# Optimization experiments

Hardware: AMD Instinct MI355X
Metric: run time of the kernel (lower is better)

Reference implementation:

```python
import jax, jax.numpy as jnp
import numpy as np

B, C, H, W = 4, 64, 512, 512
NS = 2048   # n_samples edges per image
NL = 1000   # number of superpixel labels


def setup_inputs() -> dict:
    key = jax.random.key(0)
    k1, k2, k3, k4 = jax.random.split(key, 4)
    x = jax.random.normal(k1, (B, C, H, W), dtype=jnp.float32)
    label_maps = jax.random.randint(k2, (B, 1, H, W), 0, NL).astype(jnp.int32)
    edges = jax.random.randint(k3, (B, NS, 2), 0, NL).astype(jnp.int32)
    edge_weights = (jax.random.uniform(k4, (B, NS)) > 0.5).astype(jnp.float32)
    return {"x": x, "label_maps": label_maps, "edges": edges,
            "edge_weights": edge_weights, "n_labels": NL}


def reference(x, label_maps, edges, edge_weights, n_labels):
    # x: [B,C,H,W]; label_maps: [B,1,H,W] int; edges: [B,NS,2] int; edge_weights: [B,NS]
    Bd, Cd, Hd, Wd = x.shape

    def per_image_means(xi, li):
        feats = xi.reshape(Cd, Hd * Wd).T            # [HW, C]
        lab = li.reshape(-1)                          # [HW]
        sums = jax.ops.segment_sum(feats, lab, num_segments=n_labels)   # [NL, C]
        cnts = jax.ops.segment_sum(jnp.ones((Hd * Wd,), xi.dtype), lab,
                                   num_segments=n_labels)               # [NL]
        return sums / jnp.maximum(cnts, 1)[:, None]

    means = jax.vmap(per_image_means)(x, label_maps[:, 0])  # [B, NL, C]

    bi = jnp.arange(Bd)[:, None]                  # [B,1] batch index
    xa = means[bi, edges[..., 0]]                 # [B, NS, C] mean feats at edge endpoint 0
    xb = means[bi, edges[..., 1]]                 # [B, NS, C] mean feats at edge endpoint 1
    y = edge_weights[..., None]                   # [B, NS, 1] edge weight labels
    return xa, xb, y
```

## Files before the change

### kernel.cpp

```cpp
#include <hip/hip_runtime.h>

#define Bd 4
#define Cd 64
#define HWp 262144
#define NSd 2048
#define NLd 1000

#define WIN    64
#define PXW    4096
#define NBLK   (Bd * WIN)
#define NSL    16
#define CSL    4
#define PROW   4000

typedef float __attribute__((ext_vector_type(4))) floatx4;

#define OFF_PART  0
#define OFF_BCNT  (NBLK * NSL * PROW)
#define OFF_MEANS (OFF_BCNT + NBLK * NLd)
#define WS_ELEMS  (OFF_MEANS + Bd * NLd * Cd)

__device__ __forceinline__ unsigned short f2bf(float f) {
    unsigned u = __float_as_uint(f);
    u += 0x7FFFu + ((u >> 16) & 1u);
    return (unsigned short)(u >> 16);
}
__device__ __forceinline__ unsigned pack2(float lo, float hi) {
    return ((unsigned)f2bf(hi) << 16) | (unsigned)f2bf(lo);
}
__device__ __forceinline__ float bflo(unsigned u) { return __uint_as_float(u << 16); }
__device__ __forceinline__ float bfhi(unsigned u) { return __uint_as_float(u & 0xFFFF0000u); }
__device__ __forceinline__ int clampl(int l) {
    return (l < 0) ? 0 : (l >= NLd ? NLd - 1 : l);
}

__global__ __launch_bounds__(1024, 8)
void fused_kernel(const float* __restrict__ x, const int* __restrict__ lab,
                  int* __restrict__ blockCnt, float* __restrict__ partial) {
    __shared__ int h[1024];
    __shared__ uint2 ordered[PXW];

    const int tid = threadIdx.x;
    const int g   = blockIdx.x;
    const int b   = g >> 6;
    const int win = g & 63;
    const int p0  = win * PXW;

    h[tid] = 0;
    __syncthreads();

    const int4 lv = ((const int4*)(lab + ((size_t)b << 18) + p0))[tid];
    const int l0 = clampl(lv.x), l1 = clampl(lv.y),
              l2 = clampl(lv.z), l3 = clampl(lv.w);
    atomicAdd(&h[l0], 1);
    atomicAdd(&h[l1], 1);
    atomicAdd(&h[l2], 1);
    atomicAdd(&h[l3], 1);
    __syncthreads();

    const int myCnt = h[tid];
    if (tid < NLd) blockCnt[(size_t)g * NLd + tid] = myCnt;
    for (int off = 1; off < 1024; off <<= 1) {
        int t = (tid >= off) ? h[tid - off] : 0;
        __syncthreads();
        h[tid] += t;
        __syncthreads();
    }
    const int myst = h[tid] - myCnt;
    __syncthreads();
    h[tid] = myst;
    __syncthreads();

    const int r0 = atomicAdd(&h[l0], 1) & (PXW - 1);
    const int r1 = atomicAdd(&h[l1], 1) & (PXW - 1);
    const int r2 = atomicAdd(&h[l2], 1) & (PXW - 1);
    const int r3 = atomicAdd(&h[l3], 1) & (PXW - 1);

    const float* __restrict__ xb = x + (((size_t)b * Cd) << 18) + p0 + 4 * tid;
    float* __restrict__ pout = partial + (size_t)g * NSL * PROW;

    floatx4 v0, v1, v2, v3;
    v0 = __builtin_nontemporal_load((const floatx4*)(xb + ((size_t)0 << 18)));
    v1 = __builtin_nontemporal_load((const floatx4*)(xb + ((size_t)1 << 18)));
    v2 = __builtin_nontemporal_load((const floatx4*)(xb + ((size_t)2 << 18)));
    v3 = __builtin_nontemporal_load((const floatx4*)(xb + ((size_t)3 << 18)));
    uint2 pk0, pk1, pk2, pk3;
    pk0.x = pack2(v0[0], v1[0]); pk0.y = pack2(v2[0], v3[0]);
    pk1.x = pack2(v0[1], v1[1]); pk1.y = pack2(v2[1], v3[1]);
    pk2.x = pack2(v0[2], v1[2]); pk2.y = pack2(v2[2], v3[2]);
    pk3.x = pack2(v0[3], v1[3]); pk3.y = pack2(v2[3], v3[3]);

    for (int s = 0; s < NSL; ++s) {
        __syncthreads();
        ordered[r0] = pk0;
        ordered[r1] = pk1;
        ordered[r2] = pk2;
        ordered[r3] = pk3;
        if (s + 1 < NSL) {
            const float* nb = xb + (((size_t)((s + 1) * CSL)) << 18);
            v0 = __builtin_nontemporal_load((const floatx4*)(nb + ((size_t)0 << 18)));
            v1 = __builtin_nontemporal_load((const floatx4*)(nb + ((size_t)1 << 18)));
            v2 = __builtin_nontemporal_load((const floatx4*)(nb + ((size_t)2 << 18)));
            v3 = __builtin_nontemporal_load((const floatx4*)(nb + ((size_t)3 << 18)));
        }
        __syncthreads();

        if (tid < NLd) {
            float a0 = 0, a1 = 0, a2 = 0, a3 = 0;
            for (int i = 0; i < myCnt; ++i) {
                uint2 u = ordered[(myst + i) & (PXW - 1)];
                a0 += bflo(u.x); a1 += bfhi(u.x);
                a2 += bflo(u.y); a3 += bfhi(u.y);
            }
            float4 o; o.x = a0; o.y = a1; o.z = a2; o.w = a3;
            *(float4*)(pout + (size_t)s * PROW + tid * 4) = o;
        }
        if (s + 1 < NSL) {
            pk0.x = pack2(v0[0], v1[0]); pk0.y = pack2(v2[0], v3[0]);
            pk1.x = pack2(v0[1], v1[1]); pk1.y = pack2(v2[1], v3[1]);
            pk2.x = pack2(v0[2], v1[2]); pk2.y = pack2(v2[2], v3[2]);
            pk3.x = pack2(v0[3], v1[3]); pk3.y = pack2(v2[3], v3[3]);
        }
    }
}

__global__ __launch_bounds__(256)
void combine_kernel(const float* __restrict__ partial,
                    const int* __restrict__ blockCnt,
                    float* __restrict__ means) {
    __shared__ float ninv[16];
    const int tid = threadIdx.x;
    const int b   = blockIdx.y;
    const int l0  = blockIdx.x * 16;
    const int s   = tid >> 4;
    const int ll  = tid & 15;
    const int l   = l0 + ll;

    if (tid < 16) {
        const int li = (l0 + tid < NLd) ? (l0 + tid) : (NLd - 1);
        int n = 0;
        for (int g = 0; g < WIN; ++g)
            n += blockCnt[(size_t)(b * WIN + g) * NLd + li];
        ninv[tid] = 1.0f / (float)(n > 0 ? n : 1);
    }
    __syncthreads();

    if (l < NLd) {
        float4 r; r.x = 0; r.y = 0; r.z = 0; r.w = 0;
        const float* __restrict__ pb =
            partial + (size_t)b * WIN * NSL * PROW + (size_t)s * PROW + l * 4;
        for (int g = 0; g < WIN; ++g) {
            float4 p = *(const float4*)(pb + (size_t)g * NSL * PROW);
            r.x += p.x; r.y += p.y; r.z += p.z; r.w += p.w;
        }
        const float sc = ninv[ll];
        float4 o; o.x = r.x * sc; o.y = r.y * sc; o.z = r.z * sc; o.w = r.w * sc;
        *(float4*)(means + (((size_t)(b * NLd + l)) << 6) + s * 4) = o;
    }
}

__global__ __launch_bounds__(256)
void gather_kernel(const float* __restrict__ means,
                   const int* __restrict__ edges,
                   const float* __restrict__ ew,
                   float* __restrict__ out) {
    const int t  = blockIdx.x * 256 + threadIdx.x;
    const int bs = t >> 6;
    const int c  = t & 63;
    const int b  = bs >> 11;

    const int la = clampl(edges[bs * 2 + 0]);
    const int lb = clampl(edges[bs * 2 + 1]);

    out[t] = means[((size_t)(b * NLd + la) << 6) + c];
    out[(size_t)Bd * NSd * Cd + t] = means[((size_t)(b * NLd + lb) << 6) + c];
    if (t < Bd * NSd)
        out[2 * (size_t)Bd * NSd * Cd + t] = ew[t];
}

#define WS_FB_ELEMS (Bd * Cd * NLd + Bd * NLd)

__global__ __launch_bounds__(256)
void fb_sums_kernel(const float* __restrict__ x, const int* __restrict__ lab,
                    float* __restrict__ sums) {
    __shared__ float lsum[NLd];
    const int tid   = threadIdx.x;
    const int chunk = blockIdx.x;
    const int c     = blockIdx.y;
    const int b     = blockIdx.z;

    for (int l = tid; l < NLd; l += 256) lsum[l] = 0.0f;
    __syncthreads();

    const float4* __restrict__ xp =
        (const float4*)x + (size_t)(b * Cd + c) * (HWp / 4);
    const int4* __restrict__ lp = (const int4*)lab + (size_t)b * (HWp / 4);

    const int nvec = HWp / 16;
    const int v0 = chunk * nvec, v1 = v0 + nvec;
    for (int v = v0 + tid; v < v1; v += 256) {
        float4 xv = xp[v];
        int4   lv = lp[v];
        atomicAdd(&lsum[clampl(lv.x)], xv.x);
        atomicAdd(&lsum[clampl(lv.y)], xv.y);
        atomicAdd(&lsum[clampl(lv.z)], xv.z);
        atomicAdd(&lsum[clampl(lv.w)], xv.w);
    }
    __syncthreads();

    float* __restrict__ dst = sums + (size_t)(b * Cd + c) * NLd;
    for (int l = tid; l < NLd; l += 256)
        atomicAdd(&dst[l], lsum[l]);
}

__global__ __launch_bounds__(256)
void fb_counts_kernel(const int* __restrict__ lab, float* __restrict__ counts) {
    __shared__ unsigned lcnt[NLd];
    const int tid   = threadIdx.x;
    const int chunk = blockIdx.x;
    const int b     = blockIdx.y;

    for (int l = tid; l < NLd; l += 256) lcnt[l] = 0u;
    __syncthreads();

    const int4* __restrict__ lp = (const int4*)lab + (size_t)b * (HWp / 4);
    const int nvec = HWp / 16;
    const int v0 = chunk * nvec, v1 = v0 + nvec;
    for (int v = v0 + tid; v < v1; v += 256) {
        int4 lv = lp[v];
        atomicAdd(&lcnt[clampl(lv.x)], 1u);
        atomicAdd(&lcnt[clampl(lv.y)], 1u);
        atomicAdd(&lcnt[clampl(lv.z)], 1u);
        atomicAdd(&lcnt[clampl(lv.w)], 1u);
    }
    __syncthreads();

    float* __restrict__ dst = counts + (size_t)b * NLd;
    for (int l = tid; l < NLd; l += 256)
        atomicAdd(&dst[l], (float)lcnt[l]);
}

__global__ __launch_bounds__(256)
void fb_gather_kernel(const float* __restrict__ sums,
                      const float* __restrict__ counts,
                      const int* __restrict__ edges,
                      const float* __restrict__ ew,
                      float* __restrict__ out) {
    const int t  = blockIdx.x * 256 + threadIdx.x;
    const int bs = t >> 6;
    const int c  = t & 63;
    const int b  = bs >> 11;

    const int la = clampl(edges[bs * 2 + 0]);
    const int lb = clampl(edges[bs * 2 + 1]);

    const float ca = fmaxf(counts[b * NLd + la], 1.0f);
    const float cb = fmaxf(counts[b * NLd + lb], 1.0f);

    const size_t plane = (size_t)(b * Cd + c) * NLd;
    out[t] = sums[plane + la] / ca;
    out[(size_t)Bd * NSd * Cd + t] = sums[plane + lb] / cb;
    if (t < Bd * NSd)
        out[2 * (size_t)Bd * NSd * Cd + t] = ew[t];
}

extern "C" void kernel_launch(void* const* d_in, const int* in_sizes, int n_in,
                              void* d_out, int out_size, void* d_ws, size_t ws_size,
                              hipStream_t stream) {
    const float* x     = (const float*)d_in[0];
    const int*   lab   = (const int*)d_in[1];
    const int*   edges = (const int*)d_in[2];
    const float* ew    = (const float*)d_in[3];
    float*       out   = (float*)d_out;

    const int n_gather = Bd * NSd * Cd;

    if (ws_size >= (size_t)WS_ELEMS * sizeof(float)) {
        float* partial  = (float*)d_ws + OFF_PART;
        int*   blockCnt = (int*)d_ws + OFF_BCNT;
        float* means    = (float*)d_ws + OFF_MEANS;

        fused_kernel<<<NBLK, 1024, 0, stream>>>(x, lab, blockCnt, partial);
        combine_kernel<<<dim3(63, Bd), 256, 0, stream>>>(partial, blockCnt, means);
        gather_kernel<<<n_gather / 256, 256, 0, stream>>>(means, edges, ew, out);
    } else {
        float* sums   = (float*)d_ws;
        float* counts = sums + (size_t)Bd * Cd * NLd;

        hipMemsetAsync(d_ws, 0, (size_t)WS_FB_ELEMS * sizeof(float), stream);

        fb_sums_kernel<<<dim3(4, Cd, Bd), 256, 0, stream>>>(x, lab, sums);
        fb_counts_kernel<<<dim3(4, Bd), 256, 0, stream>>>(lab, counts);
        fb_gather_kernel<<<n_gather / 256, 256, 0, stream>>>(sums, counts, edges, ew, out);
    }
}
```

Measured before the change: 86.52 us.

## Split channel slices across two blocks per window and store bf16 partial sums

The fused histogram/segment-sum kernel now launches two blocks per pixel window. Each block handles half of the channel slices, so the grid doubles to 512 blocks for better occupancy on the GPU. Per-slice partial sums are also packed to bf16 before being written to the workspace, which halves partial-write and combine-read traffic. In exchange, the label histogram and prefix scan are recomputed in both blocks, and rounding the partial sums to bf16 adds precision loss to the means.

```diff
diff --git a/kernel.cpp b/kernel.cpp
--- a/kernel.cpp
+++ b/kernel.cpp
@@ -6,18 +6,18 @@
 #define NSd 2048
 #define NLd 1000
 
-#define WIN    64
+#define NWIN   256
 #define PXW    4096
-#define NBLK   (Bd * WIN)
 #define NSL    16
 #define CSL    4
-#define PROW   4000
+#define SPB    8
+#define PU32   2000
 
 typedef float __attribute__((ext_vector_type(4))) floatx4;
 
 #define OFF_PART  0
-#define OFF_BCNT  (NBLK * NSL * PROW)
-#define OFF_MEANS (OFF_BCNT + NBLK * NLd)
+#define OFF_BCNT  (NWIN * NSL * PU32)
+#define OFF_MEANS (OFF_BCNT + NWIN * NLd)
 #define WS_ELEMS  (OFF_MEANS + Bd * NLd * Cd)
 
 __device__ __forceinline__ unsigned short f2bf(float f) {
@@ -36,15 +36,15 @@
 
 __global__ __launch_bounds__(1024, 8)
 void fused_kernel(const float* __restrict__ x, const int* __restrict__ lab,
-                  int* __restrict__ blockCnt, float* __restrict__ partial) {
+                  int* __restrict__ blockCnt, unsigned* __restrict__ partial) {
     __shared__ int h[1024];
     __shared__ uint2 ordered[PXW];
 
-    const int tid = threadIdx.x;
-    const int g   = blockIdx.x;
-    const int b   = g >> 6;
-    const int win = g & 63;
-    const int p0  = win * PXW;
+    const int tid  = threadIdx.x;
+    const int half = blockIdx.x;
+    const int w    = blockIdx.y;
+    const int b    = w >> 6;
+    const int p0   = (w & 63) * PXW;
 
     h[tid] = 0;
     __syncthreads();
@@ -59,7 +59,7 @@
     __syncthreads();
 
     const int myCnt = h[tid];
-    if (tid < NLd) blockCnt[(size_t)g * NLd + tid] = myCnt;
+    if (half == 0 && tid < NLd) blockCnt[(size_t)w * NLd + tid] = myCnt;
     for (int off = 1; off < 1024; off <<= 1) {
         int t = (tid >= off) ? h[tid - off] : 0;
         __syncthreads();
@@ -76,28 +76,30 @@
     const int r2 = atomicAdd(&h[l2], 1) & (PXW - 1);
     const int r3 = atomicAdd(&h[l3], 1) & (PXW - 1);
 
-    const float* __restrict__ xb = x + (((size_t)b * Cd) << 18) + p0 + 4 * tid;
-    float* __restrict__ pout = partial + (size_t)g * NSL * PROW;
+    const float* __restrict__ xs =
+        x + (((size_t)b * Cd + half * (SPB * CSL)) << 18) + p0 + 4 * tid;
+    unsigned* __restrict__ pout =
+        partial + ((size_t)w * NSL + half * SPB) * PU32;
 
     floatx4 v0, v1, v2, v3;
-    v0 = __builtin_nontemporal_load((const floatx4*)(xb + ((size_t)0 << 18)));
-    v1 = __builtin_nontemporal_load((const floatx4*)(xb + ((size_t)1 << 18)));
-    v2 = __builtin_nontemporal_load((const floatx4*)(xb + ((size_t)2 << 18)));
-    v3 = __builtin_nontemporal_load((const floatx4*)(xb + ((size_t)3 << 18)));
+    v0 = __builtin_nontemporal_load((const floatx4*)(xs + ((size_t)0 << 18)));
+    v1 = __builtin_nontemporal_load((const floatx4*)(xs + ((size_t)1 << 18)));
+    v2 = __builtin_nontemporal_load((const floatx4*)(xs + ((size_t)2 << 18)));
+    v3 = __builtin_nontemporal_load((const floatx4*)(xs + ((size_t)3 << 18)));
     uint2 pk0, pk1, pk2, pk3;
     pk0.x = pack2(v0[0], v1[0]); pk0.y = pack2(v2[0], v3[0]);
     pk1.x = pack2(v0[1], v1[1]); pk1.y = pack2(v2[1], v3[1]);
     pk2.x = pack2(v0[2], v1[2]); pk2.y = pack2(v2[2], v3[2]);
     pk3.x = pack2(v0[3], v1[3]); pk3.y = pack2(v2[3], v3[3]);
 
-    for (int s = 0; s < NSL; ++s) {
+    for (int s = 0; s < SPB; ++s) {
         __syncthreads();
         ordered[r0] = pk0;
         ordered[r1] = pk1;
         ordered[r2] = pk2;
         ordered[r3] = pk3;
-        if (s + 1 < NSL) {
-            const float* nb = xb + (((size_t)((s + 1) * CSL)) << 18);
+        if (s + 1 < SPB) {
+            const float* nb = xs + (((size_t)((s + 1) * CSL)) << 18);
             v0 = __builtin_nontemporal_load((const floatx4*)(nb + ((size_t)0 << 18)));
             v1 = __builtin_nontemporal_load((const floatx4*)(nb + ((size_t)1 << 18)));
             v2 = __builtin_nontemporal_load((const floatx4*)(nb + ((size_t)2 << 18)));
@@ -112,10 +114,10 @@
                 a0 += bflo(u.x); a1 += bfhi(u.x);
                 a2 += bflo(u.y); a3 += bfhi(u.y);
             }
-            float4 o; o.x = a0; o.y = a1; o.z = a2; o.w = a3;
-            *(float4*)(pout + (size_t)s * PROW + tid * 4) = o;
-        }
-        if (s + 1 < NSL) {
+            uint2 o; o.x = pack2(a0, a1); o.y = pack2(a2, a3);
+            *(uint2*)(pout + (size_t)s * PU32 + tid * 2) = o;
+        }
+        if (s + 1 < SPB) {
             pk0.x = pack2(v0[0], v1[0]); pk0.y = pack2(v2[0], v3[0]);
             pk1.x = pack2(v0[1], v1[1]); pk1.y = pack2(v2[1], v3[1]);
             pk2.x = pack2(v0[2], v1[2]); pk2.y = pack2(v2[2], v3[2]);
@@ -125,7 +127,7 @@
 }
 
 __global__ __launch_bounds__(256)
-void combine_kernel(const float* __restrict__ partial,
+void combine_kernel(const unsigned* __restrict__ partial,
                     const int* __restrict__ blockCnt,
                     float* __restrict__ means) {
     __shared__ float ninv[16];
@@ -139,22 +141,23 @@
     if (tid < 16) {
         const int li = (l0 + tid < NLd) ? (l0 + tid) : (NLd - 1);
         int n = 0;
-        for (int g = 0; g < WIN; ++g)
-            n += blockCnt[(size_t)(b * WIN + g) * NLd + li];
+        for (int g = 0; g < 64; ++g)
+            n += blockCnt[(size_t)(b * 64 + g) * NLd + li];
         ninv[tid] = 1.0f / (float)(n > 0 ? n : 1);
     }
     __syncthreads();
 
     if (l < NLd) {
-        float4 r; r.x = 0; r.y = 0; r.z = 0; r.w = 0;
-        const float* __restrict__ pb =
-            partial + (size_t)b * WIN * NSL * PROW + (size_t)s * PROW + l * 4;
-        for (int g = 0; g < WIN; ++g) {
-            float4 p = *(const float4*)(pb + (size_t)g * NSL * PROW);
-            r.x += p.x; r.y += p.y; r.z += p.z; r.w += p.w;
+        float r0 = 0, r1 = 0, r2 = 0, r3 = 0;
+        const unsigned* __restrict__ pb =
+            partial + ((size_t)(b * 64) * NSL + s) * PU32 + l * 2;
+        for (int g = 0; g < 64; ++g) {
+            uint2 p = *(const uint2*)(pb + (size_t)g * NSL * PU32);
+            r0 += bflo(p.x); r1 += bfhi(p.x);
+            r2 += bflo(p.y); r3 += bfhi(p.y);
         }
         const float sc = ninv[ll];
-        float4 o; o.x = r.x * sc; o.y = r.y * sc; o.z = r.z * sc; o.w = r.w * sc;
+        float4 o; o.x = r0 * sc; o.y = r1 * sc; o.z = r2 * sc; o.w = r3 * sc;
         *(float4*)(means + (((size_t)(b * NLd + l)) << 6) + s * 4) = o;
     }
 }
@@ -276,11 +279,11 @@
     const int n_gather = Bd * NSd * Cd;
 
     if (ws_size >= (size_t)WS_ELEMS * sizeof(float)) {
-        float* partial  = (float*)d_ws + OFF_PART;
-        int*   blockCnt = (int*)d_ws + OFF_BCNT;
-        float* means    = (float*)d_ws + OFF_MEANS;
-
-        fused_kernel<<<NBLK, 1024, 0, stream>>>(x, lab, blockCnt, partial);
+        unsigned* partial  = (unsigned*)d_ws + OFF_PART;
+        int*      blockCnt = (int*)d_ws + OFF_BCNT;
+        float*    means    = (float*)d_ws + OFF_MEANS;
+
+        fused_kernel<<<dim3(2, NWIN), 1024, 0, stream>>>(x, lab, blockCnt, partial);
         combine_kernel<<<dim3(63, Bd), 256, 0, stream>>>(partial, blockCnt, means);
         gather_kernel<<<n_gather / 256, 256, 0, stream>>>(means, edges, ew, out);
     } else {
```

After: 78.44 us, median of 2. -9.3%, faster.
